# Performance work log

Measured on AMD Instinct MI355X. Metric: run time of the kernel, lower is better.

The kernel has to match this reference:

```python
import jax, jax.numpy as jnp
import numpy as np

N = 1024
IN_F = 256
OUT_F = 128
H = 4
NH = OUT_F // H  # 32
NEG_SLOPE = 0.2


def setup_inputs() -> dict:
    key = jax.random.key(0)
    k1, k2, k3, k4, k5 = jax.random.split(key, 5)
    h = jax.random.normal(k1, (N, IN_F), dtype=jnp.float32)
    adj_mat = jax.random.randint(k2, (N, N, 1), 0, 2, dtype=jnp.int32)
    s_in = 1.0 / np.sqrt(IN_F)
    s_nh = 1.0 / np.sqrt(NH)
    Wl = jax.random.uniform(k3, (H * NH, IN_F), jnp.float32, -s_in, s_in)
    Wr = jax.random.uniform(k4, (H * NH, IN_F), jnp.float32, -s_in, s_in)
    attn_w = jax.random.uniform(k5, (NH,), jnp.float32, -s_nh, s_nh)
    return {"h": h, "adj_mat": adj_mat, "Wl": Wl, "Wr": Wr, "attn_w": attn_w}


def reference(h, adj_mat, Wl, Wr, attn_w):
    n = h.shape[0]
    g_l = (h @ Wl.T).reshape(n, H, NH)  # [N,H,F]
    g_r = (h @ Wr.T).reshape(n, H, NH)  # [N,H,F]
    # g_sum[i, j] = g_l[j] + g_r[i]  (repeat / repeat_interleave semantics)
    g_sum = g_l[None, :, :, :] + g_r[:, None, :, :]  # [N,N,H,F]
    act = jnp.where(g_sum >= 0, g_sum, NEG_SLOPE * g_sum)
    e = jnp.einsum('ijhf,f->ijh', act, attn_w)  # [N,N,H]
    mask = adj_mat != 0  # [N,N,1] broadcasts over heads
    e = jnp.where(mask, e, -jnp.inf)
    a = jax.nn.softmax(e, axis=1)  # softmax over source nodes j
    h_prime = jnp.einsum('ijh,jhf->ihf', a, g_r).reshape(n, H * NH)
    # is_output_layer=False -> ELU (dropout is a no-op in eval)
    return jax.nn.elu(h_prime)
```

## Files before the change

### kernel.cpp

```cpp
#include <hip/hip_runtime.h>
#include <math.h>

#define NN 1024
#define IN_F 256
#define OUT_F 128
#define NHEADS 4
#define NHF 32
#define HPSTR 260

__global__ void __launch_bounds__(256) glr_gemm(const float* __restrict__ hmat,
                                                const float* __restrict__ Wl,
                                                const float* __restrict__ Wr,
                                                float* __restrict__ glh,
                                                float* __restrict__ grh) {
    __shared__ float hp[64 * HPSTR];
    const int tid = threadIdx.x;
    const int rg = blockIdx.x & 15;
    const int cs = blockIdx.x >> 4;

    const float4* __restrict__ hsrc = (const float4*)hmat + rg * (64 * 64);
#pragma unroll
    for (int i = 0; i < 16; ++i) {
        const int v = tid + i * 256;
        const int row = v >> 6, kq = v & 63;
        const float4 x = hsrc[v];
        *(float4*)(hp + row * HPSTR + kq * 4) = x;
    }
    __syncthreads();

    const int lane = tid & 63;
    const int wu = __builtin_amdgcn_readfirstlane(tid >> 6);
    const int c0 = cs * 16 + wu * 4;
    const float* __restrict__ wbase = (c0 < OUT_F) ? (Wl + c0 * IN_F)
                                                   : (Wr + (c0 - OUT_F) * IN_F);
    const float* __restrict__ hrow = hp + lane * HPSTR;

    float a0 = 0.f, a1 = 0.f, a2 = 0.f, a3 = 0.f;
#pragma unroll 4
    for (int kq = 0; kq < 64; ++kq) {
        const float4 hv = *(const float4*)(hrow + kq * 4);
        const float4 w0 = *(const float4*)(wbase + 0 * IN_F + kq * 4);
        const float4 w1 = *(const float4*)(wbase + 1 * IN_F + kq * 4);
        const float4 w2 = *(const float4*)(wbase + 2 * IN_F + kq * 4);
        const float4 w3 = *(const float4*)(wbase + 3 * IN_F + kq * 4);
        a0 = fmaf(hv.x, w0.x, fmaf(hv.y, w0.y, fmaf(hv.z, w0.z, fmaf(hv.w, w0.w, a0))));
        a1 = fmaf(hv.x, w1.x, fmaf(hv.y, w1.y, fmaf(hv.z, w1.z, fmaf(hv.w, w1.w, a1))));
        a2 = fmaf(hv.x, w2.x, fmaf(hv.y, w2.y, fmaf(hv.z, w2.z, fmaf(hv.w, w2.w, a2))));
        a3 = fmaf(hv.x, w3.x, fmaf(hv.y, w3.y, fmaf(hv.z, w3.z, fmaf(hv.w, w3.w, a3))));
    }

    const int row = rg * 64 + lane;
    const int cb = c0 & (OUT_F - 1);
    const int hh = cb >> 5;
    const int f  = cb & 31;
    float* __restrict__ dst = (c0 < OUT_F) ? glh : grh;
    float4 r; r.x = a0; r.y = a1; r.z = a2; r.w = a3;
    *(float4*)(dst + (hh * NN + row) * NHF + f) = r;
}

__global__ void __launch_bounds__(512) gat_main(const float* __restrict__ glh,
                                                const float* __restrict__ grh,
                                                const int* __restrict__ adj,
                                                const float* __restrict__ attn_w,
                                                float* __restrict__ out) {
    const int hh  = blockIdx.y;
    const int i0  = blockIdx.x * 8;
    const int tid = threadIdx.x;

    __shared__ float p_buf[8][1028];
    __shared__ float part[8][16][32];
    __shared__ float red[8][8];
    __shared__ float l_sh[8];

    float lpart[8];
#pragma unroll
    for (int ii = 0; ii < 8; ++ii) lpart[ii] = 0.f;

    for (int c = 0; c < 2; ++c) {
        const int j = (c << 9) + tid;
        const float* __restrict__ gp = glh + (hh * NN + j) * NHF;
        float gl[NHF];
#pragma unroll
        for (int f4 = 0; f4 < 8; ++f4) {
            const float4 v = *(const float4*)(gp + (f4 << 2));
            gl[4 * f4 + 0] = v.x; gl[4 * f4 + 1] = v.y;
            gl[4 * f4 + 2] = v.z; gl[4 * f4 + 3] = v.w;
        }
        float alpha = 0.f;
#pragma unroll
        for (int f = 0; f < NHF; ++f) alpha = fmaf(gl[f], attn_w[f], alpha);
        int adjv[8];
#pragma unroll
        for (int ii = 0; ii < 8; ++ii) adjv[ii] = adj[(i0 + ii) * NN + j];
#pragma unroll
        for (int ii = 0; ii < 8; ++ii) {
            const float* __restrict__ grp = grh + (hh * NN + i0 + ii) * NHF;
            float S0 = 0.f, S1 = 0.f;
#pragma unroll
            for (int f = 0; f < NHF; f += 2) {
                const float s0 = gl[f]     + grp[f];
                const float s1 = gl[f + 1] + grp[f + 1];
                S0 = fmaf(fabsf(s0), attn_w[f],     S0);
                S1 = fmaf(fabsf(s1), attn_w[f + 1], S1);
            }
            const float e = fmaf(0.4f, S0 + S1, 0.6f * alpha);
            const float p = adjv[ii] ? __expf(e) : 0.f;
            p_buf[ii][j] = p;
            lpart[ii] += p;
        }
    }

    const int lane = tid & 63, wv = tid >> 6;
#pragma unroll
    for (int ii = 0; ii < 8; ++ii) {
        float v = lpart[ii];
#pragma unroll
        for (int d = 32; d > 0; d >>= 1) v += __shfl_xor(v, d);
        if (lane == 0) red[ii][wv] = v;
    }
    __syncthreads();
    if (tid < 8) {
        float l = red[tid][0];
#pragma unroll
        for (int w = 1; w < 8; ++w) l += red[tid][w];
        l_sh[tid] = l;
    }
    __syncthreads();

    const int f  = tid & 31;
    const int js = tid >> 5;
    const float* __restrict__ gp = grh + hh * NN * NHF + f;
    float o[8];
#pragma unroll
    for (int ii = 0; ii < 8; ++ii) o[ii] = 0.f;
    const int jb = js << 6;
    for (int jj = 0; jj < 64; jj += 4) {
        const int j = jb + jj;
        const float g0 = gp[(j + 0) * NHF];
        const float g1 = gp[(j + 1) * NHF];
        const float g2 = gp[(j + 2) * NHF];
        const float g3 = gp[(j + 3) * NHF];
#pragma unroll
        for (int ii = 0; ii < 8; ++ii) {
            const float4 p4 = *(const float4*)&p_buf[ii][j];
            o[ii] = fmaf(p4.x, g0, fmaf(p4.y, g1, fmaf(p4.z, g2, fmaf(p4.w, g3, o[ii]))));
        }
    }
#pragma unroll
    for (int ii = 0; ii < 8; ++ii) part[ii][js][f] = o[ii];
    __syncthreads();

    if (tid < 256) {
        const int ii = tid >> 5, ff = tid & 31;
        float s = 0.f;
#pragma unroll
        for (int k = 0; k < 16; ++k) s += part[ii][k][ff];
        s /= l_sh[ii];
        const float r = (s > 0.f) ? s : (__expf(s) - 1.f);
        out[(i0 + ii) * OUT_F + hh * NHF + ff] = r;
    }
}

extern "C" void kernel_launch(void* const* d_in, const int* in_sizes, int n_in,
                              void* d_out, int out_size, void* d_ws, size_t ws_size,
                              hipStream_t stream) {
    const float* hmat = (const float*)d_in[0];
    const int*   adj  = (const int*)d_in[1];
    const float* Wl   = (const float*)d_in[2];
    const float* Wr   = (const float*)d_in[3];
    const float* aw   = (const float*)d_in[4];
    float* o          = (float*)d_out;

    float* glh = (float*)d_ws;
    float* grh = glh + NHEADS * NN * NHF;

    glr_gemm<<<dim3(256), dim3(256), 0, stream>>>(hmat, Wl, Wr, glh, grh);
    gat_main<<<dim3(NN / 8, NHEADS), dim3(512), 0, stream>>>(glh, grh, adj, aw, o);
}
```

Measured before the change: 101.0 us.

## Restructure GEMM tiling, transpose g_l layout, packed math and LDS-staged aggregation

The projection GEMM now runs on a 2D grid with 2 output columns per wave and stages h in two K-halves, using a smaller LDS tile for more blocks. g_l is written feature-pair-major so the attention kernel's loads of it are coalesced, and the score loop uses packed 2-wide float math. The p buffer becomes j-major with 8 rows interleaved. The aggregation stages g_r tiles in LDS and reduces across lanes with shuffles instead of a shared partial-sum array. This brings more LDS traffic, more barriers and a long 32-value shuffle reduction in exchange for coalescing and packed FMA.

```diff
diff --git a/kernel.cpp b/kernel.cpp
--- a/kernel.cpp
+++ b/kernel.cpp
@@ -1,113 +1,121 @@
 #include <hip/hip_runtime.h>
 #include <math.h>
+
+typedef float v2f __attribute__((ext_vector_type(2)));
 
 #define NN 1024
 #define IN_F 256
 #define OUT_F 128
 #define NHEADS 4
 #define NHF 32
-#define HPSTR 260
 
 __global__ void __launch_bounds__(256) glr_gemm(const float* __restrict__ hmat,
                                                 const float* __restrict__ Wl,
                                                 const float* __restrict__ Wr,
-                                                float* __restrict__ glh,
+                                                v2f* __restrict__ glT,
                                                 float* __restrict__ grh) {
-    __shared__ float hp[64 * HPSTR];
-    const int tid = threadIdx.x;
-    const int rg = blockIdx.x & 15;
-    const int cs = blockIdx.x >> 4;
-
-    const float4* __restrict__ hsrc = (const float4*)hmat + rg * (64 * 64);
-#pragma unroll
-    for (int i = 0; i < 16; ++i) {
-        const int v = tid + i * 256;
-        const int row = v >> 6, kq = v & 63;
-        const float4 x = hsrc[v];
-        *(float4*)(hp + row * HPSTR + kq * 4) = x;
-    }
-    __syncthreads();
-
+    __shared__ float hs[64 * 132];
+    const int tid  = threadIdx.x;
+    const int rg   = blockIdx.x;
+    const int cs   = blockIdx.y;
     const int lane = tid & 63;
-    const int wu = __builtin_amdgcn_readfirstlane(tid >> 6);
-    const int c0 = cs * 16 + wu * 4;
-    const float* __restrict__ wbase = (c0 < OUT_F) ? (Wl + c0 * IN_F)
-                                                   : (Wr + (c0 - OUT_F) * IN_F);
-    const float* __restrict__ hrow = hp + lane * HPSTR;
-
-    float a0 = 0.f, a1 = 0.f, a2 = 0.f, a3 = 0.f;
-#pragma unroll 4
-    for (int kq = 0; kq < 64; ++kq) {
-        const float4 hv = *(const float4*)(hrow + kq * 4);
-        const float4 w0 = *(const float4*)(wbase + 0 * IN_F + kq * 4);
-        const float4 w1 = *(const float4*)(wbase + 1 * IN_F + kq * 4);
-        const float4 w2 = *(const float4*)(wbase + 2 * IN_F + kq * 4);
-        const float4 w3 = *(const float4*)(wbase + 3 * IN_F + kq * 4);
-        a0 = fmaf(hv.x, w0.x, fmaf(hv.y, w0.y, fmaf(hv.z, w0.z, fmaf(hv.w, w0.w, a0))));
-        a1 = fmaf(hv.x, w1.x, fmaf(hv.y, w1.y, fmaf(hv.z, w1.z, fmaf(hv.w, w1.w, a1))));
-        a2 = fmaf(hv.x, w2.x, fmaf(hv.y, w2.y, fmaf(hv.z, w2.z, fmaf(hv.w, w2.w, a2))));
-        a3 = fmaf(hv.x, w3.x, fmaf(hv.y, w3.y, fmaf(hv.z, w3.z, fmaf(hv.w, w3.w, a3))));
+    const int wu   = __builtin_amdgcn_readfirstlane(tid >> 6);
+    const int c0   = cs * 8 + wu * 2;
+    const int half = c0 >> 7;
+    const int cc   = c0 & 127;
+    const float* __restrict__ W   = half ? Wr : Wl;
+    const float* __restrict__ wr0 = W + cc * IN_F;
+    const float* __restrict__ wr1 = wr0 + IN_F;
+
+    float a0 = 0.f, a1 = 0.f;
+    for (int kh = 0; kh < 2; ++kh) {
+#pragma unroll
+        for (int s = 0; s < 8; ++s) {
+            const int v = tid + s * 256;
+            const int row = v >> 5, q = v & 31;
+            const float4 x = ((const float4*)hmat)[(rg * 64 + row) * 64 + kh * 32 + q];
+            *(float4*)(hs + row * 132 + q * 4) = x;
+        }
+        __syncthreads();
+        const float4* __restrict__ w0p = (const float4*)(wr0 + kh * 128);
+        const float4* __restrict__ w1p = (const float4*)(wr1 + kh * 128);
+        const float*  __restrict__ hrow = hs + lane * 132;
+#pragma unroll 8
+        for (int q = 0; q < 32; ++q) {
+            const float4 hv = *(const float4*)(hrow + q * 4);
+            const float4 w0 = w0p[q];
+            const float4 w1 = w1p[q];
+            a0 = fmaf(hv.x, w0.x, fmaf(hv.y, w0.y, fmaf(hv.z, w0.z, fmaf(hv.w, w0.w, a0))));
+            a1 = fmaf(hv.x, w1.x, fmaf(hv.y, w1.y, fmaf(hv.z, w1.z, fmaf(hv.w, w1.w, a1))));
+        }
+        __syncthreads();
     }
 
     const int row = rg * 64 + lane;
-    const int cb = c0 & (OUT_F - 1);
-    const int hh = cb >> 5;
-    const int f  = cb & 31;
-    float* __restrict__ dst = (c0 < OUT_F) ? glh : grh;
-    float4 r; r.x = a0; r.y = a1; r.z = a2; r.w = a3;
-    *(float4*)(dst + (hh * NN + row) * NHF + f) = r;
+    const int hh = cc >> 5, f0 = cc & 31;
+    if (half == 0) {
+        glT[(hh * 16 + (f0 >> 1)) * NN + row] = (v2f){a0, a1};
+    } else {
+        *(v2f*)(grh + (hh * NN + row) * NHF + f0) = (v2f){a0, a1};
+    }
 }
 
-__global__ void __launch_bounds__(512) gat_main(const float* __restrict__ glh,
-                                                const float* __restrict__ grh,
-                                                const int* __restrict__ adj,
-                                                const float* __restrict__ attn_w,
-                                                float* __restrict__ out) {
+__global__ void __launch_bounds__(512, 4) gat_main(const v2f* __restrict__ glT,
+                                                   const float* __restrict__ grh,
+                                                   const int* __restrict__ adj,
+                                                   const float* __restrict__ attn_w,
+                                                   float* __restrict__ out) {
     const int hh  = blockIdx.y;
     const int i0  = blockIdx.x * 8;
     const int tid = threadIdx.x;
 
-    __shared__ float p_buf[8][1028];
-    __shared__ float part[8][16][32];
+    __shared__ float p_buf[NN * 12];
+    __shared__ float g_t[128 * 36];
     __shared__ float red[8][8];
     __shared__ float l_sh[8];
 
+    const v2f* __restrict__ w2p = (const v2f*)attn_w;
+
     float lpart[8];
 #pragma unroll
     for (int ii = 0; ii < 8; ++ii) lpart[ii] = 0.f;
 
     for (int c = 0; c < 2; ++c) {
         const int j = (c << 9) + tid;
-        const float* __restrict__ gp = glh + (hh * NN + j) * NHF;
-        float gl[NHF];
-#pragma unroll
-        for (int f4 = 0; f4 < 8; ++f4) {
-            const float4 v = *(const float4*)(gp + (f4 << 2));
-            gl[4 * f4 + 0] = v.x; gl[4 * f4 + 1] = v.y;
-            gl[4 * f4 + 2] = v.z; gl[4 * f4 + 3] = v.w;
-        }
-        float alpha = 0.f;
-#pragma unroll
-        for (int f = 0; f < NHF; ++f) alpha = fmaf(gl[f], attn_w[f], alpha);
+        const v2f* __restrict__ glp = glT + hh * 16 * NN + j;
+        v2f gl2[16];
+#pragma unroll
+        for (int fp = 0; fp < 16; ++fp) gl2[fp] = glp[fp * NN];
+
+        v2f aa = {0.f, 0.f};
+#pragma unroll
+        for (int fp = 0; fp < 16; ++fp) aa += gl2[fp] * w2p[fp];
+        const float alpha6 = 0.6f * (aa.x + aa.y);
+
         int adjv[8];
 #pragma unroll
         for (int ii = 0; ii < 8; ++ii) adjv[ii] = adj[(i0 + ii) * NN + j];
+
+        float pv[8];
 #pragma unroll
         for (int ii = 0; ii < 8; ++ii) {
-            const float* __restrict__ grp = grh + (hh * NN + i0 + ii) * NHF;
-            float S0 = 0.f, S1 = 0.f;
-#pragma unroll
-            for (int f = 0; f < NHF; f += 2) {
-                const float s0 = gl[f]     + grp[f];
-                const float s1 = gl[f + 1] + grp[f + 1];
-                S0 = fmaf(fabsf(s0), attn_w[f],     S0);
-                S1 = fmaf(fabsf(s1), attn_w[f + 1], S1);
+            const v2f* __restrict__ gr2 = (const v2f*)(grh + (hh * NN + i0 + ii) * NHF);
+            v2f S = {0.f, 0.f};
+#pragma unroll
+            for (int fp = 0; fp < 16; ++fp) {
+                const v2f s = gl2[fp] + gr2[fp];
+                const v2f m = __builtin_elementwise_max(s, -s);
+                S += m * w2p[fp];
             }
-            const float e = fmaf(0.4f, S0 + S1, 0.6f * alpha);
+            const float e = fmaf(0.4f, S.x + S.y, alpha6);
             const float p = adjv[ii] ? __expf(e) : 0.f;
-            p_buf[ii][j] = p;
+            pv[ii] = p;
             lpart[ii] += p;
         }
+        float4 wA; wA.x = pv[0]; wA.y = pv[1]; wA.z = pv[2]; wA.w = pv[3];
+        float4 wB; wB.x = pv[4]; wB.y = pv[5]; wB.z = pv[6]; wB.w = pv[7];
+        *(float4*)&p_buf[j * 12]     = wA;
+        *(float4*)&p_buf[j * 12 + 4] = wB;
     }
 
     const int lane = tid & 63, wv = tid >> 6;
@@ -127,37 +135,66 @@
     }
     __syncthreads();
 
-    const int f  = tid & 31;
-    const int js = tid >> 5;
-    const float* __restrict__ gp = grh + hh * NN * NHF + f;
-    float o[8];
-#pragma unroll
-    for (int ii = 0; ii < 8; ++ii) o[ii] = 0.f;
-    const int jb = js << 6;
-    for (int jj = 0; jj < 64; jj += 4) {
-        const int j = jb + jj;
-        const float g0 = gp[(j + 0) * NHF];
-        const float g1 = gp[(j + 1) * NHF];
-        const float g2 = gp[(j + 2) * NHF];
-        const float g3 = gp[(j + 3) * NHF];
+    v2f acc[8][2];
+#pragma unroll
+    for (int ii = 0; ii < 8; ++ii) { acc[ii][0] = (v2f){0.f, 0.f}; acc[ii][1] = (v2f){0.f, 0.f}; }
+
+    for (int t = 0; t < 8; ++t) {
+        const float4* __restrict__ src = (const float4*)(grh + (hh * NN + t * 128) * NHF);
+#pragma unroll
+        for (int s2 = 0; s2 < 2; ++s2) {
+            const int u = tid + s2 * 512;
+            const int jj = u >> 3, f4 = u & 7;
+            const float4 x = src[u];
+            *(float4*)&g_t[jj * 36 + f4 * 4] = x;
+        }
+        __syncthreads();
+#pragma unroll
+        for (int u2 = 0; u2 < 2; ++u2) {
+            const int jl = lane + (u2 << 6);
+            const float* __restrict__ pb = &p_buf[(t * 128 + jl) * 12];
+            const float4 pA = *(const float4*)pb;
+            const float4 pB = *(const float4*)(pb + 4);
+            const float4 g  = *(const float4*)&g_t[jl * 36 + wv * 4];
+            const v2f g01 = {g.x, g.y}, g23 = {g.z, g.w};
+            acc[0][0] += (v2f){pA.x, pA.x} * g01;  acc[0][1] += (v2f){pA.x, pA.x} * g23;
+            acc[1][0] += (v2f){pA.y, pA.y} * g01;  acc[1][1] += (v2f){pA.y, pA.y} * g23;
+            acc[2][0] += (v2f){pA.z, pA.z} * g01;  acc[2][1] += (v2f){pA.z, pA.z} * g23;
+            acc[3][0] += (v2f){pA.w, pA.w} * g01;  acc[3][1] += (v2f){pA.w, pA.w} * g23;
+            acc[4][0] += (v2f){pB.x, pB.x} * g01;  acc[4][1] += (v2f){pB.x, pB.x} * g23;
+            acc[5][0] += (v2f){pB.y, pB.y} * g01;  acc[5][1] += (v2f){pB.y, pB.y} * g23;
+            acc[6][0] += (v2f){pB.z, pB.z} * g01;  acc[6][1] += (v2f){pB.z, pB.z} * g23;
+            acc[7][0] += (v2f){pB.w, pB.w} * g01;  acc[7][1] += (v2f){pB.w, pB.w} * g23;
+        }
+        __syncthreads();
+    }
+
+    float o32[32];
+#pragma unroll
+    for (int ii = 0; ii < 8; ++ii) {
+        o32[ii * 4 + 0] = acc[ii][0].x;  o32[ii * 4 + 1] = acc[ii][0].y;
+        o32[ii * 4 + 2] = acc[ii][1].x;  o32[ii * 4 + 3] = acc[ii][1].y;
+    }
+#pragma unroll
+    for (int d = 32; d > 0; d >>= 1) {
+#pragma unroll
+        for (int k = 0; k < 32; ++k) o32[k] += __shfl_xor(o32[k], d);
+    }
+    if (lane == 0) {
 #pragma unroll
         for (int ii = 0; ii < 8; ++ii) {
-            const float4 p4 = *(const float4*)&p_buf[ii][j];
-            o[ii] = fmaf(p4.x, g0, fmaf(p4.y, g1, fmaf(p4.z, g2, fmaf(p4.w, g3, o[ii]))));
-        }
-    }
-#pragma unroll
-    for (int ii = 0; ii < 8; ++ii) part[ii][js][f] = o[ii];
-    __syncthreads();
-
-    if (tid < 256) {
-        const int ii = tid >> 5, ff = tid & 31;
-        float s = 0.f;
-#pragma unroll
-        for (int k = 0; k < 16; ++k) s += part[ii][k][ff];
-        s /= l_sh[ii];
-        const float r = (s > 0.f) ? s : (__expf(s) - 1.f);
-        out[(i0 + ii) * OUT_F + hh * NHF + ff] = r;
+            const float inv = 1.f / l_sh[ii];
+            float x0 = o32[ii * 4 + 0] * inv;
+            float x1 = o32[ii * 4 + 1] * inv;
+            float x2 = o32[ii * 4 + 2] * inv;
+            float x3 = o32[ii * 4 + 3] * inv;
+            float4 r;
+            r.x = (x0 > 0.f) ? x0 : (__expf(x0) - 1.f);
+            r.y = (x1 > 0.f) ? x1 : (__expf(x1) - 1.f);
+            r.z = (x2 > 0.f) ? x2 : (__expf(x2) - 1.f);
+            r.w = (x3 > 0.f) ? x3 : (__expf(x3) - 1.f);
+            *(float4*)(out + (i0 + ii) * OUT_F + hh * NHF + wv * 4) = r;
+        }
     }
 }
 
@@ -171,9 +208,10 @@
     const float* aw   = (const float*)d_in[4];
     float* o          = (float*)d_out;
 
-    float* glh = (float*)d_ws;
-    float* grh = glh + NHEADS * NN * NHF;
-
-    glr_gemm<<<dim3(256), dim3(256), 0, stream>>>(hmat, Wl, Wr, glh, grh);
-    gat_main<<<dim3(NN / 8, NHEADS), dim3(512), 0, stream>>>(glh, grh, adj, aw, o);
+    float* wsf = (float*)d_ws;
+    v2f*   glT = (v2f*)wsf;
+    float* grh = wsf + NHEADS * 16 * NN * 2;
+
+    glr_gemm<<<dim3(16, 32), dim3(256), 0, stream>>>(hmat, Wl, Wr, glT, grh);
+    gat_main<<<dim3(NN / 8, NHEADS), dim3(512), 0, stream>>>(glT, grh, adj, aw, o);
 }
```

Result: slower. 107.5 us (+6.4%).
